# Kernel tuning notes

Hardware: AMD Instinct MI355X
Metric: run time of the kernel (lower is better)

The kernel has to match this reference:

```python
import jax, jax.numpy as jnp
import numpy as np
import math

THETA = 10000.0
NUM_HEADS = 16


def _rope(x, pos, theta):
    # x: [B, H, S, d_k], pos: [S] int
    d_k = x.shape[-1]
    inv_freq = 1.0 / (theta ** (jnp.arange(0, d_k, 2, dtype=jnp.float32) / d_k))  # [d_k/2]
    freqs = pos.astype(jnp.float32)[:, None] * inv_freq[None, :]  # [S, d_k/2]
    cos = jnp.cos(freqs)  # broadcast over B, H
    sin = jnp.sin(freqs)
    x_even = x[..., 0::2]
    x_odd = x[..., 1::2]
    r_even = x_even * cos - x_odd * sin
    r_odd = x_even * sin + x_odd * cos
    # interleave back: [..., S, d_k/2, 2] -> [..., S, d_k]
    return jnp.stack([r_even, r_odd], axis=-1).reshape(x.shape)


def setup_inputs() -> dict:
    key = jax.random.key(0)
    ks = jax.random.split(key, 5)
    B, S, D = 2, 2048, 1024
    sigma = math.sqrt(2.0 / (D + D))
    return {
        "x": jax.random.normal(ks[0], (B, S, D), dtype=jnp.float32),
        "Wq": jax.random.normal(ks[1], (D, D), dtype=jnp.float32) * sigma,
        "Wk": jax.random.normal(ks[2], (D, D), dtype=jnp.float32) * sigma,
        "Wv": jax.random.normal(ks[3], (D, D), dtype=jnp.float32) * sigma,
        "Wo": jax.random.normal(ks[4], (D, D), dtype=jnp.float32) * sigma,
        "token_positions": jnp.arange(S, dtype=jnp.int32),
    }


def reference(x, Wq, Wk, Wv, Wo, token_positions):
    B, S, D = x.shape
    H = NUM_HEADS
    d_k = D // H

    def split_heads(t):  # [B,S,D] -> [B,H,S,d_k]
        return t.reshape(B, S, H, d_k).transpose(0, 2, 1, 3)

    q = split_heads(x @ Wq.T)
    k = split_heads(x @ Wk.T)
    v = split_heads(x @ Wv.T)

    q = _rope(q, token_positions, THETA)
    k = _rope(k, token_positions, THETA)

    scores = jnp.einsum("bhqd,bhkd->bhqk", q, k) / jnp.sqrt(jnp.float32(d_k))
    causal = jnp.tril(jnp.ones((S, S), dtype=bool))
    scores = jnp.where(causal, scores, jnp.finfo(scores.dtype).min)
    probs = jax.nn.softmax(scores, axis=-1)
    attn = jnp.einsum("bhqk,bhkd->bhqd", probs, v)  # [B,H,S,d_k]

    attn = attn.transpose(0, 2, 1, 3).reshape(B, S, D)
    return attn @ Wo.T
```

## Files before the change

### kernel.cpp

```cpp
#include <hip/hip_runtime.h>
#include <hip/hip_bf16.h>

#define B_ 2
#define S_ 2048
#define D_ 1024
#define H_ 16
#define DK_ 64
#define M_ (B_*S_)
#define K_ D_

typedef __attribute__((ext_vector_type(8))) short bf16x8;
typedef __attribute__((ext_vector_type(4))) float f32x4;

__device__ __forceinline__ unsigned short f2bf(float f) {
  unsigned u = __float_as_uint(f);
  u += 0x7fff + ((u >> 16) & 1);
  return (unsigned short)(u >> 16);
}

__device__ __forceinline__ void gload_lds16(const void* g, void* l) {
  __builtin_amdgcn_global_load_lds(
      (const __attribute__((address_space(1))) unsigned int*)(unsigned long long)g,
      (__attribute__((address_space(3))) unsigned int*)(unsigned int)(unsigned long long)l,
      16, 0, 0);
}

__global__ __launch_bounds__(256) void k_cvt(
    const float* __restrict__ x,
    const float* __restrict__ w0, const float* __restrict__ w1,
    const float* __restrict__ w2, const float* __restrict__ w3,
    unsigned short* __restrict__ xb, unsigned short* __restrict__ wb,
    const int* __restrict__ pos, float2* __restrict__ tab) {
  const int bid = blockIdx.x;
  if (bid >= 8192) {
    int t = (bid - 8192) * 256 + threadIdx.x;
    int s = t >> 5, j = t & 31;
    float inv = powf(10000.0f, -(float)j / 32.0f);
    float ang = (float)pos[s] * inv;
    tab[t] = make_float2(cosf(ang), sinf(ang));
    return;
  }
  const float* sp;
  unsigned short* dp;
  size_t off;
  if (bid < 4096) {
    sp = x; dp = xb; off = (size_t)bid * 1024 + threadIdx.x * 4;
  } else {
    const int wi = (bid - 4096) >> 10;
    sp = (wi == 0) ? w0 : (wi == 1) ? w1 : (wi == 2) ? w2 : w3;
    dp = wb + (size_t)wi * D_ * K_;
    off = (size_t)((bid - 4096) & 1023) * 1024 + threadIdx.x * 4;
  }
  float4 v = *(const float4*)(sp + off);
  ushort4 o;
  o.x = f2bf(v.x); o.y = f2bf(v.y); o.z = f2bf(v.z); o.w = f2bf(v.w);
  *(ushort4*)(dp + off) = o;
}

__global__ __launch_bounds__(256, 2) void k_gemm0(
    const unsigned short* __restrict__ A,
    const unsigned short* __restrict__ Wall,
    unsigned short* __restrict__ qkv,
    const float2* __restrict__ tab)
{
  __shared__ unsigned short SA[2][128*32];
  __shared__ unsigned short SB[2][192*32];
  const int tid = threadIdx.x, lane = tid & 63, w = tid >> 6;
  const int wr = w >> 1, wc = w & 1;
  const int c = lane & 15, hg = lane >> 4;
  const int m0 = blockIdx.x * 128;
  const int n0 = blockIdx.y * 192;
  const unsigned short* Ag = A + (size_t)m0 * K_;
  const unsigned short* Bg = Wall + (size_t)n0 * K_;

  f32x4 acc[4][6];
#pragma unroll
  for (int m = 0; m < 4; ++m)
#pragma unroll
    for (int n = 0; n < 6; ++n) acc[m][n] = (f32x4){0.f, 0.f, 0.f, 0.f};

  const int sr = (lane >> 2);
  const int sc = (lane & 3) * 8;

#define GS0(KT, BI)                                                           \
  do {                                                                        \
    _Pragma("unroll")                                                         \
    for (int cc = 0; cc < 2; ++cc)                                            \
      gload_lds16(Ag + (size_t)(w*32 + cc*16 + sr)*K_ + (KT) + sc,            \
                  &SA[BI][(w*32 + cc*16)*32]);                                \
    _Pragma("unroll")                                                         \
    for (int bb = 0; bb < 3; ++bb)                                            \
      gload_lds16(Bg + (size_t)(w*48 + bb*16 + sr)*K_ + (KT) + sc,            \
                  &SB[BI][(w*48 + bb*16)*32]);                                \
  } while (0)

  GS0(0, 0);
  for (int t = 0; t < K_/32; ++t) {
    asm volatile("s_waitcnt vmcnt(0)" ::: "memory");
    __builtin_amdgcn_s_barrier();
    asm volatile("" ::: "memory");
    if (t + 1 < K_/32) GS0((t+1)*32, (t & 1) ^ 1);

    const int bi = t & 1;
    bf16x8 af[4], bfr[6];
#pragma unroll
    for (int m = 0; m < 4; ++m)
      af[m] = *(const bf16x8*)&SA[bi][(wr*64 + m*16 + c)*32 + hg*8];
#pragma unroll
    for (int n = 0; n < 6; ++n)
      bfr[n] = *(const bf16x8*)&SB[bi][(wc*96 + n*16 + c)*32 + hg*8];
#pragma unroll
    for (int m = 0; m < 4; ++m)
#pragma unroll
      for (int n = 0; n < 6; ++n)
        acc[m][n] = __builtin_amdgcn_mfma_f32_16x16x32_bf16(af[m], bfr[n], acc[m][n], 0, 0, 0);
  }
#undef GS0

#pragma unroll
  for (int m = 0; m < 4; ++m)
#pragma unroll
    for (int n = 0; n < 6; ++n) {
      const int row0 = m0 + wr*64 + m*16 + hg*4;
      const int col  = n0 + wc*96 + n*16 + c;
      const int z = col >> 10;
      const int colz = col & 1023;
      const int h = colz >> 6, d = colz & 63;
      unsigned short* dst = qkv + (size_t)z * M_ * D_;
      if (z == 2) {
        const int b = row0 >> 11, s0 = row0 & (S_ - 1);
        ushort4 o;
        o.x = f2bf(acc[m][n][0]); o.y = f2bf(acc[m][n][1]);
        o.z = f2bf(acc[m][n][2]); o.w = f2bf(acc[m][n][3]);
        *(ushort4*)&dst[((size_t)(b*H_ + h)*DK_ + d)*S_ + s0] = o;
      } else {
        const float post = (z == 0) ? 0.18033688f : 1.0f;
        const float sgn = (d & 1) ? 1.0f : -1.0f;
#pragma unroll
        for (int r = 0; r < 4; ++r) {
          const int row = row0 + r;
          const int b = row >> 11, s = row & (S_ - 1);
          float v  = acc[m][n][r];
          float pv = __shfl_xor(v, 1);
          float2 cs = tab[s*32 + (d >> 1)];
          float ov = (v * cs.x + sgn * pv * cs.y) * post;
          dst[((size_t)(b*H_ + h)*S_ + s)*DK_ + d] = f2bf(ov);
        }
      }
    }
}

__global__ __launch_bounds__(256) void k_gemm1(
    const unsigned short* __restrict__ A,
    const unsigned short* __restrict__ Wo,
    float* __restrict__ fout)
{
  __shared__ unsigned short As[2][64*32];
  __shared__ unsigned short Bs[2][128*32];
  const int tid = threadIdx.x, lane = tid & 63, w = tid >> 6;
  const int wr = w >> 1, wc = w & 1;
  const int c = lane & 15, hg = lane >> 4;
  const int m0 = blockIdx.x * 64, n0 = blockIdx.y * 128;
  const unsigned short* Ag = A + (size_t)m0 * K_;
  const unsigned short* Bg = Wo + (size_t)n0 * K_;

  f32x4 acc[2][4];
#pragma unroll
  for (int m = 0; m < 2; ++m)
#pragma unroll
    for (int n = 0; n < 4; ++n) acc[m][n] = (f32x4){0.f, 0.f, 0.f, 0.f};

  const int sr = (lane >> 2);
  const int sc = (lane & 3) * 8;

#define GS1(KT, BI)                                                           \
  do {                                                                        \
    gload_lds16(Ag + (size_t)(w*16 + sr)*K_ + (KT) + sc,                      \
                &As[BI][(w*16)*32]);                                          \
    _Pragma("unroll")                                                         \
    for (int cc = 0; cc < 2; ++cc)                                            \
      gload_lds16(Bg + (size_t)(w*32 + cc*16 + sr)*K_ + (KT) + sc,            \
                  &Bs[BI][(w*32 + cc*16)*32]);                                \
  } while (0)

  GS1(0, 0);
  for (int t = 0; t < K_/32; ++t) {
    asm volatile("s_waitcnt vmcnt(0)" ::: "memory");
    __builtin_amdgcn_s_barrier();
    asm volatile("" ::: "memory");
    if (t + 1 < K_/32) GS1((t+1)*32, (t & 1) ^ 1);

    const int bi = t & 1;
    bf16x8 af[2], bfr[4];
#pragma unroll
    for (int m = 0; m < 2; ++m)
      af[m] = *(const bf16x8*)&As[bi][(wr*32 + m*16 + c)*32 + hg*8];
#pragma unroll
    for (int n = 0; n < 4; ++n)
      bfr[n] = *(const bf16x8*)&Bs[bi][(wc*64 + n*16 + c)*32 + hg*8];
#pragma unroll
    for (int m = 0; m < 2; ++m)
#pragma unroll
      for (int n = 0; n < 4; ++n)
        acc[m][n] = __builtin_amdgcn_mfma_f32_16x16x32_bf16(af[m], bfr[n], acc[m][n], 0, 0, 0);
  }
#undef GS1

#pragma unroll
  for (int m = 0; m < 2; ++m)
#pragma unroll
    for (int n = 0; n < 4; ++n) {
      const int row0 = m0 + wr*32 + m*16 + hg*4;
      const int col  = n0 + wc*64 + n*16 + c;
#pragma unroll
      for (int r = 0; r < 4; ++r)
        fout[(size_t)(row0 + r)*D_ + col] = acc[m][n][r];
    }
}

__global__ __launch_bounds__(256) void k_attn(
    const unsigned short* __restrict__ Qg,
    const unsigned short* __restrict__ Kg,
    const unsigned short* __restrict__ Vtg,
    unsigned short* __restrict__ Og)
{
  __shared__ unsigned short Kb[3][64*64];
  __shared__ unsigned short Vb[3][64*64];
  __shared__ unsigned short Ps[4][32*72];

  const int tid = threadIdx.x, lane = tid & 63, w = tid >> 6;
  const int bid = blockIdx.x;
  const int xcd = bid & 7, idx = bid >> 3;
  const int head = xcd * 4 + (idx & 3);
  const int p  = idx >> 2;
  const int hv = 31 - p;
  const int c = lane & 15, hg = lane >> 4;
  const int q0m[2] = { hv*64 + w*16, p*64 + w*16 };

  const unsigned short* Qp = Qg + (size_t)head * S_ * DK_;
  const unsigned short* Kp = Kg + (size_t)head * S_ * DK_;
  const unsigned short* Vp = Vtg + (size_t)head * DK_ * S_;

  const int srow   = w*8 + (lane >> 3);
  const int schunk = (lane & 7) ^ (lane >> 3);

  const short ONE_BF = (short)0x3F80;
  const bf16x8 vones = {ONE_BF, ONE_BF, ONE_BF, ONE_BF, ONE_BF, ONE_BF, ONE_BF, ONE_BF};
  const f32x4 NEG8 = {-8.f, -8.f, -8.f, -8.f};

  bf16x8 aq[2][2];
#pragma unroll
  for (int m = 0; m < 2; ++m)
#pragma unroll
    for (int kk = 0; kk < 2; ++kk)
      aq[m][kk] = *(const bf16x8*)(Qp + (size_t)(q0m[m] + c)*DK_ + kk*32 + hg*8);

  f32x4 oacc[2][4], lacc[2];
#pragma unroll
  for (int m = 0; m < 2; ++m) {
#pragma unroll
    for (int n = 0; n < 4; ++n) oacc[m][n] = (f32x4){0.f, 0.f, 0.f, 0.f};
    lacc[m] = (f32x4){0.f, 0.f, 0.f, 0.f};
  }

  const int nkv = hv + 1;

#define STAGE(T, BI)                                                          \
  do {                                                                        \
    const int kv0s = (T) * 64;                                                \
    _Pragma("unroll")                                                         \
    for (int i = 0; i < 2; ++i) {                                             \
      gload_lds16(Kp + (size_t)(kv0s + i*32 + srow)*DK_ + schunk*8,           \
                  &Kb[BI][(i*32 + w*8)*64]);                                  \
      gload_lds16(Vp + (size_t)(i*32 + srow)*S_ + kv0s + schunk*8,            \
                  &Vb[BI][(i*32 + w*8)*64]);                                  \
    }                                                                         \
  } while (0)

  STAGE(0, 0);
  if (nkv > 1) STAGE(1, 1);

  int cb = 0;
  for (int t = 0; t < nkv; ++t) {
    if (t + 1 < nkv) { asm volatile("s_waitcnt vmcnt(4)" ::: "memory"); }
    else             { asm volatile("s_waitcnt vmcnt(0)" ::: "memory"); }
    __builtin_amdgcn_s_barrier();
    asm volatile("" ::: "memory");
    if (t + 2 < nkv) {
      int sb = cb + 2; if (sb >= 3) sb -= 3;
      STAGE(t + 2, sb);
    }

    const int kv0 = t * 64;
    const bool live1 = (t <= p);

    bf16x8 bk[4][2];
#pragma unroll
    for (int n = 0; n < 4; ++n)
#pragma unroll
      for (int kk = 0; kk < 2; ++kk)
        bk[n][kk] = *(const bf16x8*)&Kb[cb][(n*16 + c)*64 + (((kk*4 + hg) ^ (c & 7))*8)];

    f32x4 sc4[2][4];
    __builtin_amdgcn_s_setprio(1);
#pragma unroll
    for (int m = 0; m < 2; ++m) {
      if (m == 1 && !live1) break;
#pragma unroll
      for (int n = 0; n < 4; ++n) {
        sc4[m][n] = __builtin_amdgcn_mfma_f32_16x16x32_bf16(bk[n][0], aq[m][0], NEG8, 0, 0, 0);
        sc4[m][n] = __builtin_amdgcn_mfma_f32_16x16x32_bf16(bk[n][1], aq[m][1], sc4[m][n], 0, 0, 0);
      }
    }
    __builtin_amdgcn_s_setprio(0);

    bf16x8 bv[4][2];
#pragma unroll
    for (int n = 0; n < 4; ++n)
#pragma unroll
      for (int kk = 0; kk < 2; ++kk)
        bv[n][kk] = *(const bf16x8*)&Vb[cb][(n*16 + c)*64 + (((kk*4 + hg) ^ (c & 7))*8)];

#pragma unroll
    for (int m = 0; m < 2; ++m) {
      if (m == 1 && !live1) continue;
      const int tm = (m == 0) ? hv : p;
      const int qg = q0m[m] + c;
      if (t == tm) {
#pragma unroll
        for (int n = 0; n < 4; ++n)
#pragma unroll
          for (int r = 0; r < 4; ++r)
            if (kv0 + n*16 + hg*4 + r > qg) sc4[m][n][r] = -INFINITY;
      }

#pragma unroll
      for (int n = 0; n < 4; ++n) {
        union { __hip_bfloat162 h2[2]; ushort4 u; } pk;
        pk.h2[0] = __float22bfloat162_rn(
            make_float2(exp2f(sc4[m][n][0]), exp2f(sc4[m][n][1])));
        pk.h2[1] = __float22bfloat162_rn(
            make_float2(exp2f(sc4[m][n][2]), exp2f(sc4[m][n][3])));
        *(ushort4*)&Ps[w][(m*16 + c)*72 + n*16 + hg*4] = pk.u;
      }

      bf16x8 ap[2];
#pragma unroll
      for (int kk = 0; kk < 2; ++kk)
        ap[kk] = *(const bf16x8*)&Ps[w][(m*16 + c)*72 + kk*32 + hg*8];
      __builtin_amdgcn_s_setprio(1);
#pragma unroll
      for (int n = 0; n < 4; ++n)
#pragma unroll
        for (int kk = 0; kk < 2; ++kk)
          oacc[m][n] = __builtin_amdgcn_mfma_f32_16x16x32_bf16(ap[kk], bv[n][kk], oacc[m][n], 0, 0, 0);
#pragma unroll
      for (int kk = 0; kk < 2; ++kk)
        lacc[m] = __builtin_amdgcn_mfma_f32_16x16x32_bf16(ap[kk], vones, lacc[m], 0, 0, 0);
      __builtin_amdgcn_s_setprio(0);
    }

    asm volatile("" ::: "memory");
    if (++cb == 3) cb = 0;
  }
#undef STAGE

  const int b = head >> 4, h = head & 15;
#pragma unroll
  for (int m = 0; m < 2; ++m) {
    float rl[4];
#pragma unroll
    for (int r = 0; r < 4; ++r) rl[r] = 1.0f / lacc[m][r];
#pragma unroll
    for (int n = 0; n < 4; ++n)
#pragma unroll
      for (int r = 0; r < 4; ++r) {
        const int s = q0m[m] + hg*4 + r;
        const int d = n*16 + c;
        Og[((size_t)b*S_ + s)*D_ + h*DK_ + d] = f2bf(oacc[m][n][r] * rl[r]);
      }
  }
}

extern "C" void kernel_launch(void* const* d_in, const int* in_sizes, int n_in,
                              void* d_out, int out_size, void* d_ws, size_t ws_size,
                              hipStream_t stream) {
  const float* x = (const float*)d_in[0];
  const float* Wm[4] = {(const float*)d_in[1], (const float*)d_in[2],
                        (const float*)d_in[3], (const float*)d_in[4]};
  const int* tp = (const int*)d_in[5];
  float* out = (float*)d_out;

  unsigned short* ws = (unsigned short*)d_ws;
  const size_t MD = (size_t)M_ * D_;
  unsigned short* xb  = ws;
  unsigned short* wb  = ws + MD;
  unsigned short* qws = ws + MD + 4*(size_t)D_*K_;
  float2* tab = (float2*)(ws + MD + 4*(size_t)D_*K_ + 3*MD);

  k_cvt<<<dim3(8448), 256, 0, stream>>>(x, Wm[0], Wm[1], Wm[2], Wm[3], xb, wb, tp, tab);

  k_gemm0<<<dim3(M_/128, 16), 256, 0, stream>>>(xb, wb, qws, tab);

  unsigned short* attn = xb;
  k_attn<<<dim3(512), 256, 0, stream>>>(qws, qws + MD, qws + 2*MD, attn);

  k_gemm1<<<dim3(M_/64, D_/128), 256, 0, stream>>>(attn, wb + 3*(size_t)D_*K_, out);
}
```

Before: 106.9 us.

## Deepen QKV GEMM k-tile with swizzled LDS and unroll attention ring buffer

The QKV projection GEMM now stages 64-wide k-tiles instead of 32, using an XOR-swizzled LDS layout, and runs two MFMA sub-steps per barrier. This halves the number of barrier/wait iterations and aims to avoid LDS bank conflicts, at the cost of twice the shared memory, which may limit occupancy. The attention loop is unrolled by three so the triple-buffer indices become compile-time constants. It also uses the raw exp2 builtin, which skips the library's denormal handling. STAGE(1,1) is now issued even when nkv is 1, which may prefetch an unused tile.

```diff
diff --git a/kernel.cpp b/kernel.cpp
--- a/kernel.cpp
+++ b/kernel.cpp
@@ -63,8 +63,8 @@
     unsigned short* __restrict__ qkv,
     const float2* __restrict__ tab)
 {
-  __shared__ unsigned short SA[2][128*32];
-  __shared__ unsigned short SB[2][192*32];
+  __shared__ unsigned short SA[2][128*64];
+  __shared__ unsigned short SB[2][192*64];
   const int tid = threadIdx.x, lane = tid & 63, w = tid >> 6;
   const int wr = w >> 1, wc = w & 1;
   const int c = lane & 15, hg = lane >> 4;
@@ -79,41 +79,44 @@
 #pragma unroll
     for (int n = 0; n < 6; ++n) acc[m][n] = (f32x4){0.f, 0.f, 0.f, 0.f};
 
-  const int sr = (lane >> 2);
-  const int sc = (lane & 3) * 8;
+  const int srow   = w*8 + (lane >> 3);
+  const int schunk = (lane & 7) ^ (lane >> 3);
 
 #define GS0(KT, BI)                                                           \
   do {                                                                        \
     _Pragma("unroll")                                                         \
-    for (int cc = 0; cc < 2; ++cc)                                            \
-      gload_lds16(Ag + (size_t)(w*32 + cc*16 + sr)*K_ + (KT) + sc,            \
-                  &SA[BI][(w*32 + cc*16)*32]);                                \
-    _Pragma("unroll")                                                         \
-    for (int bb = 0; bb < 3; ++bb)                                            \
-      gload_lds16(Bg + (size_t)(w*48 + bb*16 + sr)*K_ + (KT) + sc,            \
-                  &SB[BI][(w*48 + bb*16)*32]);                                \
+    for (int i = 0; i < 4; ++i)                                               \
+      gload_lds16(Ag + (size_t)(i*32 + srow)*K_ + (KT) + schunk*8,            \
+                  &SA[BI][(i*32 + w*8)*64]);                                  \
+    _Pragma("unroll")                                                         \
+    for (int i = 0; i < 6; ++i)                                               \
+      gload_lds16(Bg + (size_t)(i*32 + srow)*K_ + (KT) + schunk*8,            \
+                  &SB[BI][(i*32 + w*8)*64]);                                  \
   } while (0)
 
   GS0(0, 0);
-  for (int t = 0; t < K_/32; ++t) {
+  for (int t = 0; t < K_/64; ++t) {
     asm volatile("s_waitcnt vmcnt(0)" ::: "memory");
     __builtin_amdgcn_s_barrier();
     asm volatile("" ::: "memory");
-    if (t + 1 < K_/32) GS0((t+1)*32, (t & 1) ^ 1);
+    if (t + 1 < K_/64) GS0((t+1)*64, (t & 1) ^ 1);
 
     const int bi = t & 1;
-    bf16x8 af[4], bfr[6];
-#pragma unroll
-    for (int m = 0; m < 4; ++m)
-      af[m] = *(const bf16x8*)&SA[bi][(wr*64 + m*16 + c)*32 + hg*8];
-#pragma unroll
-    for (int n = 0; n < 6; ++n)
-      bfr[n] = *(const bf16x8*)&SB[bi][(wc*96 + n*16 + c)*32 + hg*8];
-#pragma unroll
-    for (int m = 0; m < 4; ++m)
+#pragma unroll
+    for (int kk = 0; kk < 2; ++kk) {
+      bf16x8 af[4], bfr[6];
+#pragma unroll
+      for (int m = 0; m < 4; ++m)
+        af[m] = *(const bf16x8*)&SA[bi][(wr*64 + m*16 + c)*64 + (((kk*4 + hg) ^ (c & 7))*8)];
 #pragma unroll
       for (int n = 0; n < 6; ++n)
-        acc[m][n] = __builtin_amdgcn_mfma_f32_16x16x32_bf16(af[m], bfr[n], acc[m][n], 0, 0, 0);
+        bfr[n] = *(const bf16x8*)&SB[bi][(wc*96 + n*16 + c)*64 + (((kk*4 + hg) ^ (c & 7))*8)];
+#pragma unroll
+      for (int m = 0; m < 4; ++m)
+#pragma unroll
+        for (int n = 0; n < 6; ++n)
+          acc[m][n] = __builtin_amdgcn_mfma_f32_16x16x32_bf16(af[m], bfr[n], acc[m][n], 0, 0, 0);
+    }
   }
 #undef GS0
 
@@ -277,92 +280,93 @@
     }                                                                         \
   } while (0)
 
+#define ABODY(TT, CB, SB)                                                     \
+  {                                                                           \
+    const int t = (TT);                                                       \
+    if (t + 1 < nkv) { asm volatile("s_waitcnt vmcnt(4)" ::: "memory"); }     \
+    else             { asm volatile("s_waitcnt vmcnt(0)" ::: "memory"); }     \
+    __builtin_amdgcn_s_barrier();                                             \
+    asm volatile("" ::: "memory");                                            \
+    if (t + 2 < nkv) STAGE(t + 2, SB);                                        \
+    const int kv0 = t * 64;                                                   \
+    const bool live1 = (t <= p);                                              \
+    bf16x8 bk[4][2];                                                          \
+    _Pragma("unroll")                                                         \
+    for (int n = 0; n < 4; ++n)                                               \
+      _Pragma("unroll")                                                       \
+      for (int kk = 0; kk < 2; ++kk)                                          \
+        bk[n][kk] = *(const bf16x8*)&Kb[CB][(n*16 + c)*64 + (((kk*4 + hg) ^ (c & 7))*8)]; \
+    f32x4 sc4[2][4];                                                          \
+    __builtin_amdgcn_s_setprio(1);                                            \
+    _Pragma("unroll")                                                         \
+    for (int m = 0; m < 2; ++m) {                                             \
+      if (m == 1 && !live1) break;                                            \
+      _Pragma("unroll")                                                       \
+      for (int n = 0; n < 4; ++n) {                                           \
+        sc4[m][n] = __builtin_amdgcn_mfma_f32_16x16x32_bf16(bk[n][0], aq[m][0], NEG8, 0, 0, 0); \
+        sc4[m][n] = __builtin_amdgcn_mfma_f32_16x16x32_bf16(bk[n][1], aq[m][1], sc4[m][n], 0, 0, 0); \
+      }                                                                       \
+    }                                                                         \
+    __builtin_amdgcn_s_setprio(0);                                            \
+    bf16x8 bv[4][2];                                                          \
+    _Pragma("unroll")                                                         \
+    for (int n = 0; n < 4; ++n)                                               \
+      _Pragma("unroll")                                                       \
+      for (int kk = 0; kk < 2; ++kk)                                          \
+        bv[n][kk] = *(const bf16x8*)&Vb[CB][(n*16 + c)*64 + (((kk*4 + hg) ^ (c & 7))*8)]; \
+    _Pragma("unroll")                                                         \
+    for (int m = 0; m < 2; ++m) {                                             \
+      if (m == 1 && !live1) continue;                                         \
+      const int tm = (m == 0) ? hv : p;                                       \
+      const int qg = q0m[m] + c;                                              \
+      if (t == tm) {                                                          \
+        _Pragma("unroll")                                                     \
+        for (int n = 0; n < 4; ++n)                                           \
+          _Pragma("unroll")                                                   \
+          for (int r = 0; r < 4; ++r)                                         \
+            if (kv0 + n*16 + hg*4 + r > qg) sc4[m][n][r] = -INFINITY;         \
+      }                                                                       \
+      _Pragma("unroll")                                                       \
+      for (int n = 0; n < 4; ++n) {                                           \
+        union { __hip_bfloat162 h2[2]; ushort4 u; } pk;                       \
+        pk.h2[0] = __float22bfloat162_rn(make_float2(                         \
+            __builtin_amdgcn_exp2f(sc4[m][n][0]),                             \
+            __builtin_amdgcn_exp2f(sc4[m][n][1])));                           \
+        pk.h2[1] = __float22bfloat162_rn(make_float2(                         \
+            __builtin_amdgcn_exp2f(sc4[m][n][2]),                             \
+            __builtin_amdgcn_exp2f(sc4[m][n][3])));                           \
+        *(ushort4*)&Ps[w][(m*16 + c)*72 + n*16 + hg*4] = pk.u;                \
+      }                                                                       \
+      bf16x8 ap[2];                                                           \
+      _Pragma("unroll")                                                       \
+      for (int kk = 0; kk < 2; ++kk)                                          \
+        ap[kk] = *(const bf16x8*)&Ps[w][(m*16 + c)*72 + kk*32 + hg*8];        \
+      __builtin_amdgcn_s_setprio(1);                                          \
+      _Pragma("unroll")                                                       \
+      for (int n = 0; n < 4; ++n)                                             \
+        _Pragma("unroll")                                                     \
+        for (int kk = 0; kk < 2; ++kk)                                        \
+          oacc[m][n] = __builtin_amdgcn_mfma_f32_16x16x32_bf16(ap[kk], bv[n][kk], oacc[m][n], 0, 0, 0); \
+      _Pragma("unroll")                                                       \
+      for (int kk = 0; kk < 2; ++kk)                                          \
+        lacc[m] = __builtin_amdgcn_mfma_f32_16x16x32_bf16(ap[kk], vones, lacc[m], 0, 0, 0); \
+      __builtin_amdgcn_s_setprio(0);                                          \
+    }                                                                         \
+    asm volatile("" ::: "memory");                                            \
+  }
+
   STAGE(0, 0);
-  if (nkv > 1) STAGE(1, 1);
-
-  int cb = 0;
-  for (int t = 0; t < nkv; ++t) {
-    if (t + 1 < nkv) { asm volatile("s_waitcnt vmcnt(4)" ::: "memory"); }
-    else             { asm volatile("s_waitcnt vmcnt(0)" ::: "memory"); }
-    __builtin_amdgcn_s_barrier();
-    asm volatile("" ::: "memory");
-    if (t + 2 < nkv) {
-      int sb = cb + 2; if (sb >= 3) sb -= 3;
-      STAGE(t + 2, sb);
-    }
-
-    const int kv0 = t * 64;
-    const bool live1 = (t <= p);
-
-    bf16x8 bk[4][2];
-#pragma unroll
-    for (int n = 0; n < 4; ++n)
-#pragma unroll
-      for (int kk = 0; kk < 2; ++kk)
-        bk[n][kk] = *(const bf16x8*)&Kb[cb][(n*16 + c)*64 + (((kk*4 + hg) ^ (c & 7))*8)];
-
-    f32x4 sc4[2][4];
-    __builtin_amdgcn_s_setprio(1);
-#pragma unroll
-    for (int m = 0; m < 2; ++m) {
-      if (m == 1 && !live1) break;
-#pragma unroll
-      for (int n = 0; n < 4; ++n) {
-        sc4[m][n] = __builtin_amdgcn_mfma_f32_16x16x32_bf16(bk[n][0], aq[m][0], NEG8, 0, 0, 0);
-        sc4[m][n] = __builtin_amdgcn_mfma_f32_16x16x32_bf16(bk[n][1], aq[m][1], sc4[m][n], 0, 0, 0);
-      }
-    }
-    __builtin_amdgcn_s_setprio(0);
-
-    bf16x8 bv[4][2];
-#pragma unroll
-    for (int n = 0; n < 4; ++n)
-#pragma unroll
-      for (int kk = 0; kk < 2; ++kk)
-        bv[n][kk] = *(const bf16x8*)&Vb[cb][(n*16 + c)*64 + (((kk*4 + hg) ^ (c & 7))*8)];
-
-#pragma unroll
-    for (int m = 0; m < 2; ++m) {
-      if (m == 1 && !live1) continue;
-      const int tm = (m == 0) ? hv : p;
-      const int qg = q0m[m] + c;
-      if (t == tm) {
-#pragma unroll
-        for (int n = 0; n < 4; ++n)
-#pragma unroll
-          for (int r = 0; r < 4; ++r)
-            if (kv0 + n*16 + hg*4 + r > qg) sc4[m][n][r] = -INFINITY;
-      }
-
-#pragma unroll
-      for (int n = 0; n < 4; ++n) {
-        union { __hip_bfloat162 h2[2]; ushort4 u; } pk;
-        pk.h2[0] = __float22bfloat162_rn(
-            make_float2(exp2f(sc4[m][n][0]), exp2f(sc4[m][n][1])));
-        pk.h2[1] = __float22bfloat162_rn(
-            make_float2(exp2f(sc4[m][n][2]), exp2f(sc4[m][n][3])));
-        *(ushort4*)&Ps[w][(m*16 + c)*72 + n*16 + hg*4] = pk.u;
-      }
-
-      bf16x8 ap[2];
-#pragma unroll
-      for (int kk = 0; kk < 2; ++kk)
-        ap[kk] = *(const bf16x8*)&Ps[w][(m*16 + c)*72 + kk*32 + hg*8];
-      __builtin_amdgcn_s_setprio(1);
-#pragma unroll
-      for (int n = 0; n < 4; ++n)
-#pragma unroll
-        for (int kk = 0; kk < 2; ++kk)
-          oacc[m][n] = __builtin_amdgcn_mfma_f32_16x16x32_bf16(ap[kk], bv[n][kk], oacc[m][n], 0, 0, 0);
-#pragma unroll
-      for (int kk = 0; kk < 2; ++kk)
-        lacc[m] = __builtin_amdgcn_mfma_f32_16x16x32_bf16(ap[kk], vones, lacc[m], 0, 0, 0);
-      __builtin_amdgcn_s_setprio(0);
-    }
-
-    asm volatile("" ::: "memory");
-    if (++cb == 3) cb = 0;
-  }
+  STAGE(1, 1);
+
+  int t3 = 0;
+  for (; t3 + 3 <= nkv; t3 += 3) {
+    ABODY(t3,     0, 2)
+    ABODY(t3 + 1, 1, 0)
+    ABODY(t3 + 2, 2, 1)
+  }
+  if (t3 < nkv)     { ABODY(t3,     0, 2) }
+  if (t3 + 1 < nkv) { ABODY(t3 + 1, 1, 0) }
+#undef ABODY
 #undef STAGE
 
   const int b = head >> 4, h = head & 15;
```

Measured after the change: 109.3 us. 2.2% more time.

## Widen QKV GEMM K-tile to 64 with XOR-swizzled LDS, use raw exp2 intrinsic

Applied to the files above, without the earlier changes.

The QKV projection GEMM now stages K-slices of 64 instead of 32 per pipeline step. The LDS tiles are reorganised with an XOR swizzle on 16-byte chunks so fragment reads avoid bank conflicts. This halves the number of barrier/waitcnt iterations, at the cost of doubling shared memory per block, which may limit occupancy. Separately, the attention softmax replaces exp2f with the hardware exp2 builtin, which skips the library's range and denormal handling.

```diff
diff --git a/kernel.cpp b/kernel.cpp
--- a/kernel.cpp
+++ b/kernel.cpp
@@ -63,8 +63,8 @@
     unsigned short* __restrict__ qkv,
     const float2* __restrict__ tab)
 {
-  __shared__ unsigned short SA[2][128*32];
-  __shared__ unsigned short SB[2][192*32];
+  __shared__ unsigned short SA[2][128*64];
+  __shared__ unsigned short SB[2][192*64];
   const int tid = threadIdx.x, lane = tid & 63, w = tid >> 6;
   const int wr = w >> 1, wc = w & 1;
   const int c = lane & 15, hg = lane >> 4;
@@ -79,41 +79,44 @@
 #pragma unroll
     for (int n = 0; n < 6; ++n) acc[m][n] = (f32x4){0.f, 0.f, 0.f, 0.f};
 
-  const int sr = (lane >> 2);
-  const int sc = (lane & 3) * 8;
+  const int srow   = w*8 + (lane >> 3);
+  const int schunk = (lane & 7) ^ (lane >> 3);
 
 #define GS0(KT, BI)                                                           \
   do {                                                                        \
     _Pragma("unroll")                                                         \
-    for (int cc = 0; cc < 2; ++cc)                                            \
-      gload_lds16(Ag + (size_t)(w*32 + cc*16 + sr)*K_ + (KT) + sc,            \
-                  &SA[BI][(w*32 + cc*16)*32]);                                \
+    for (int i = 0; i < 4; ++i)                                               \
+      gload_lds16(Ag + (size_t)(i*32 + srow)*K_ + (KT) + schunk*8,            \
+                  &SA[BI][(i*32 + w*8)*64]);                                  \
     _Pragma("unroll")                                                         \
-    for (int bb = 0; bb < 3; ++bb)                                            \
-      gload_lds16(Bg + (size_t)(w*48 + bb*16 + sr)*K_ + (KT) + sc,            \
-                  &SB[BI][(w*48 + bb*16)*32]);                                \
+    for (int i = 0; i < 6; ++i)                                               \
+      gload_lds16(Bg + (size_t)(i*32 + srow)*K_ + (KT) + schunk*8,            \
+                  &SB[BI][(i*32 + w*8)*64]);                                  \
   } while (0)
 
   GS0(0, 0);
-  for (int t = 0; t < K_/32; ++t) {
+  for (int t = 0; t < K_/64; ++t) {
     asm volatile("s_waitcnt vmcnt(0)" ::: "memory");
     __builtin_amdgcn_s_barrier();
     asm volatile("" ::: "memory");
-    if (t + 1 < K_/32) GS0((t+1)*32, (t & 1) ^ 1);
+    if (t + 1 < K_/64) GS0((t+1)*64, (t & 1) ^ 1);
 
     const int bi = t & 1;
-    bf16x8 af[4], bfr[6];
-#pragma unroll
-    for (int m = 0; m < 4; ++m)
-      af[m] = *(const bf16x8*)&SA[bi][(wr*64 + m*16 + c)*32 + hg*8];
-#pragma unroll
-    for (int n = 0; n < 6; ++n)
-      bfr[n] = *(const bf16x8*)&SB[bi][(wc*96 + n*16 + c)*32 + hg*8];
-#pragma unroll
-    for (int m = 0; m < 4; ++m)
+#pragma unroll
+    for (int kk = 0; kk < 2; ++kk) {
+      bf16x8 af[4], bfr[6];
+#pragma unroll
+      for (int m = 0; m < 4; ++m)
+        af[m] = *(const bf16x8*)&SA[bi][(wr*64 + m*16 + c)*64 + (((kk*4 + hg) ^ (c & 7))*8)];
 #pragma unroll
       for (int n = 0; n < 6; ++n)
-        acc[m][n] = __builtin_amdgcn_mfma_f32_16x16x32_bf16(af[m], bfr[n], acc[m][n], 0, 0, 0);
+        bfr[n] = *(const bf16x8*)&SB[bi][(wc*96 + n*16 + c)*64 + (((kk*4 + hg) ^ (c & 7))*8)];
+#pragma unroll
+      for (int m = 0; m < 4; ++m)
+#pragma unroll
+        for (int n = 0; n < 6; ++n)
+          acc[m][n] = __builtin_amdgcn_mfma_f32_16x16x32_bf16(af[m], bfr[n], acc[m][n], 0, 0, 0);
+    }
   }
 #undef GS0
 
@@ -337,10 +340,12 @@
 #pragma unroll
       for (int n = 0; n < 4; ++n) {
         union { __hip_bfloat162 h2[2]; ushort4 u; } pk;
-        pk.h2[0] = __float22bfloat162_rn(
-            make_float2(exp2f(sc4[m][n][0]), exp2f(sc4[m][n][1])));
-        pk.h2[1] = __float22bfloat162_rn(
-            make_float2(exp2f(sc4[m][n][2]), exp2f(sc4[m][n][3])));
+        pk.h2[0] = __float22bfloat162_rn(make_float2(
+            __builtin_amdgcn_exp2f(sc4[m][n][0]),
+            __builtin_amdgcn_exp2f(sc4[m][n][1])));
+        pk.h2[1] = __float22bfloat162_rn(make_float2(
+            __builtin_amdgcn_exp2f(sc4[m][n][2]),
+            __builtin_amdgcn_exp2f(sc4[m][n][3])));
         *(ushort4*)&Ps[w][(m*16 + c)*72 + n*16 + hg*4] = pk.u;
       }
 
```

New measurement: 97.73 us. -8.6%, faster.
